# Kernel tuning notes

Hardware: AMD Instinct MI355X
Metric: run time of the kernel (lower is better)

## Reference

```python
import jax, jax.numpy as jnp
import numpy as np

N_NODES = 100000
N_EDGES = 1600000
D_IN = 64
D_OUT = 64
K_PLUS = 3
ALPHA = 0.5
EXPONENT = -0.25


def _dir_norm_edge_weights(row, col, n, exponent):
    # directed_norm: D_out^exp A D_in^exp, zero-degree -> 0 weight
    ones = jnp.ones(row.shape[0], dtype=jnp.float32)
    out_deg = jax.ops.segment_sum(ones, row, num_segments=n)
    in_deg = jax.ops.segment_sum(ones, col, num_segments=n)
    out_inv = jnp.where(out_deg > 0, jnp.power(jnp.maximum(out_deg, 1.0), exponent), 0.0)
    in_inv = jnp.where(in_deg > 0, jnp.power(jnp.maximum(in_deg, 1.0), exponent), 0.0)
    return out_inv[row] * in_inv[col]


def _spmm(w, x, out_idx, gather_idx, n):
    # y[out_idx] += w * x[gather_idx]
    return jax.ops.segment_sum(w[:, None] * x[gather_idx], out_idx, num_segments=n)


def setup_inputs() -> dict:
    key = jax.random.key(0)
    ks = jax.random.split(key, 7)
    x_real = jax.random.normal(ks[0], (N_NODES, D_IN), dtype=jnp.float32)
    x_imag = jax.random.normal(ks[1], (N_NODES, D_IN), dtype=jnp.float32)
    edge_index = jax.random.randint(ks[2], (2, N_EDGES), 0, N_NODES, dtype=jnp.int32)
    s = 1.0 / np.sqrt(D_IN)
    W_real = jax.random.normal(ks[3], (K_PLUS, D_OUT, D_IN), dtype=jnp.float32) * s
    b_real = jax.random.normal(ks[4], (K_PLUS, D_OUT), dtype=jnp.float32) * s
    W_imag = jax.random.normal(ks[5], (K_PLUS, D_OUT, D_IN), dtype=jnp.float32) * s
    b_imag = jax.random.normal(ks[6], (K_PLUS, D_OUT), dtype=jnp.float32) * s
    return {"x_real": x_real, "x_imag": x_imag, "edge_index": edge_index,
            "W_real": W_real, "b_real": b_real, "W_imag": W_imag, "b_imag": b_imag}


def reference(x_real, x_imag, edge_index, W_real, b_real, W_imag, b_imag):
    n = x_real.shape[0]
    row, col = edge_index[0], edge_index[1]
    # adj_norm edge weights; adj_t_norm weights are identical scalars per edge
    # (in/out degrees swap under transpose), only the scatter direction differs.
    w = _dir_norm_edge_weights(row, col, n, EXPONENT)

    y_real = _spmm(w, x_real, row, col, n)    # adj_norm @ x_real
    y_imag = _spmm(w, x_imag, row, col, n)    # adj_norm @ x_imag
    y_real_t = _spmm(w, x_real, col, row, n)  # adj_t_norm @ x_real
    y_imag_t = _spmm(w, x_imag, col, row, n)  # adj_t_norm @ x_imag

    def lin_r(y):  # [K, N, O] per-order real linear
        return jnp.einsum('nd,kod->kno', y, W_real) + b_real[:, None, :]

    def lin_i(y):
        return jnp.einsum('nd,kod->kno', y, W_imag) + b_imag[:, None, :]

    coeffs = (0.5 ** jnp.arange(K_PLUS, dtype=jnp.float32))[:, None, None]  # exp penalty, i=0 -> 1

    lr_yr, li_yr = lin_r(y_real), lin_i(y_real)
    lr_yi, li_yi = lin_r(y_imag), lin_i(y_imag)
    lr_yrt, li_yrt = lin_r(y_real_t), lin_i(y_real_t)
    lr_yit, li_yit = lin_r(y_imag_t), lin_i(y_imag_t)

    sum_real_s2d = jnp.sum((lr_yr - li_yi) * coeffs, axis=0)
    sum_imag_s2d = jnp.sum((li_yr + lr_yi) * coeffs, axis=0)
    sum_real_d2s = jnp.sum((lr_yrt - li_yit) * coeffs, axis=0)
    # NOTE: faithful to original source, which uses y_real (not y_real_t) here.
    sum_imag_d2s = jnp.sum((li_yr + lr_yit) * coeffs, axis=0)

    total_real = ALPHA * sum_real_s2d + (1.0 - ALPHA) * sum_real_d2s
    total_imag = ALPHA * sum_imag_s2d + (1.0 - ALPHA) * sum_imag_d2s
    return total_real, total_imag
```

## Files before the change

### kernel.cpp

```cpp
#include <hip/hip_runtime.h>
#include <hip/hip_fp16.h>


constexpr int D = 64;
constexpr int G1 = 256;

typedef _Float16 f16x8 __attribute__((ext_vector_type(8)));
typedef float f32x4 __attribute__((ext_vector_type(4)));

__device__ __forceinline__ float2 h2_to_f2(uint p) {
  __half2 h = *(__half2*)&p;
  return __half22float2(h);
}


__global__ __launch_bounds__(256) void part_count(
    const int* __restrict__ row, const int* __restrict__ col,
    int* __restrict__ Tcnt, int E, int NBUK, int CH) {
  __shared__ int ho[256], hi_[256];
  int t = threadIdx.x, g = blockIdx.x;
  ho[t] = 0;
  hi_[t] = 0;
  __syncthreads();
  int e0 = g * CH, e1 = min(E, e0 + CH);
  for (int e = e0 + t; e < e1; e += 256) {
    atomicAdd(&ho[row[e] >> 9], 1);
    atomicAdd(&hi_[col[e] >> 9], 1);
  }
  __syncthreads();
  if (t < NBUK) {
    if (ho[t]) atomicAdd(&Tcnt[t], ho[t]);
    if (hi_[t]) atomicAdd(&Tcnt[NBUK + t], hi_[t]);
  }
}

__global__ __launch_bounds__(1024) void prep_kernel(
    const float* __restrict__ Wr, const float* __restrict__ br,
    const float* __restrict__ Wi, const float* __restrict__ bi,
    const int* __restrict__ Tcnt, uint4* __restrict__ Bfrag,
    float* __restrict__ cR, float* __restrict__ cI,
    int* __restrict__ Bb_out, int* __restrict__ Bb_in, int* __restrict__ Ccur,
    int E, int NBUK) {
  __shared__ uint sWh[4096];
  __shared__ int ws[8];
  int t = threadIdx.x;
  for (int i = t; i < 4096; i += 1024) {
    int o = i >> 6, d = i & 63;
    float wr = Wr[i] + 0.5f * Wr[4096 + i] + 0.25f * Wr[8192 + i];
    float wi = Wi[i] + 0.5f * Wi[4096 + i] + 0.25f * Wi[8192 + i];
    __half2 h = __floats2half2_rn(wr, wi);
    sWh[d * 64 + o] = *(uint*)&h;
  }
  if (t < 64) {
    float brv = br[t] + 0.5f * br[64 + t] + 0.25f * br[128 + t];
    float biv = bi[t] + 0.5f * bi[64 + t] + 0.25f * bi[128 + t];
    cR[t] = brv - biv;
    cI[t] = brv + biv;
  }
  int dir = 0, tl = 0, v = 0, sc = 0;
  int lane = t & 63, wv = t >> 6;
  if (t < 512) {
    dir = t >> 8;
    tl = t & 255;
    v = (tl < NBUK) ? Tcnt[dir * NBUK + tl] : 0;
    sc = v;
#pragma unroll
    for (int off = 1; off < 64; off <<= 1) {
      int u = __shfl_up(sc, off);
      if (lane >= off) sc += u;
    }
    if (lane == 63) ws[wv] = sc;
  }
  __syncthreads();
  if (t < 512) {
    int wbase = 0;
#pragma unroll
    for (int w = 0; w < 8; ++w)
      if (w >= (dir << 2) && w < wv) wbase += ws[w];
    int excl = wbase + sc - v;
    int* Bb = dir ? Bb_in : Bb_out;
    if (tl < NBUK) {
      Bb[tl] = excl;
      Ccur[dir * NBUK + tl] = excl;
      if (tl == NBUK - 1) Bb[NBUK] = excl + v;
    }
  }
  for (int tt = t; tt < 2048; tt += 1024) {
    int ln = tt & 63, fr = tt >> 6;
    int mat = fr >> 4, kt = (fr >> 2) & 3, nt = fr & 3;
    int o = (ln & 15) + 16 * nt;
    int k0 = 8 * (ln >> 4) + 32 * kt;
    uint wbits[4];
#pragma unroll
    for (int jj = 0; jj < 4; ++jj) {
      float vv[2];
#pragma unroll
      for (int s = 0; s < 2; ++s) {
        int k = k0 + 2 * jj + s;
        float2 wrwi = h2_to_f2(sWh[(k & 63) * 64 + o]);
        vv[s] = (k < 64) ? wrwi.x : (mat ? wrwi.y : -wrwi.y);
      }
      __half2 hh = __floats2half2_rn(vv[0], vv[1]);
      wbits[jj] = *(uint*)&hh;
    }
    Bfrag[tt] = make_uint4(wbits[0], wbits[1], wbits[2], wbits[3]);
  }
}

__global__ __launch_bounds__(256) void part_scatter(
    const int* __restrict__ row, const int* __restrict__ col,
    int* __restrict__ Ccur,
    uint* __restrict__ pout, uint* __restrict__ pin, int E, int NBUK, int CH) {
  __shared__ int co[256], ci[256];
  int t = threadIdx.x, g = blockIdx.x;
  co[t] = 0;
  ci[t] = 0;
  __syncthreads();
  int e0 = g * CH, e1 = min(E, e0 + CH);
  for (int e = e0 + t; e < e1; e += 256) {
    atomicAdd(&co[row[e] >> 9], 1);
    atomicAdd(&ci[col[e] >> 9], 1);
  }
  __syncthreads();
  if (t < NBUK) {
    int c = co[t];
    co[t] = c ? atomicAdd(&Ccur[t], c) : 0;
    c = ci[t];
    ci[t] = c ? atomicAdd(&Ccur[NBUK + t], c) : 0;
  }
  __syncthreads();
  for (int e = e0 + t; e < e1; e += 256) {
    int r = row[e], c = col[e];
    int po = atomicAdd(&co[r >> 9], 1);
    pout[po] = ((uint)(r & 511) << 17) | (uint)c;
    int pi = atomicAdd(&ci[c >> 9], 1);
    pin[pi] = ((uint)(c & 511) << 17) | (uint)r;
  }
}

__global__ __launch_bounds__(256) void offsets_kernel(
    const uint* __restrict__ pout, const uint* __restrict__ pin,
    const int* __restrict__ Bb_out, const int* __restrict__ Bb_in,
    int* __restrict__ ofs_out, int* __restrict__ ofs_in,
    float* __restrict__ inv_out, float* __restrict__ inv_in,
    int E, int NBUK, int N) {
  const uint* p = blockIdx.y ? pin : pout;
  const int* Bb = blockIdx.y ? Bb_in : Bb_out;
  int* ofs = blockIdx.y ? ofs_in : ofs_out;
  float* inv = blockIdx.y ? inv_in : inv_out;
  __shared__ int ld[512];
  __shared__ int ws[4];
  int t = threadIdx.x, b = blockIdx.x;
  ld[t] = 0;
  ld[t + 256] = 0;
  __syncthreads();
  int win_s = Bb[b], win_e = Bb[b + 1];
  for (int j = win_s + t; j < win_e; j += 256) atomicAdd(&ld[p[j] >> 17], 1);
  __syncthreads();
  int a0 = ld[2 * t], a1 = ld[2 * t + 1], sm = a0 + a1;
  int lane = t & 63, wv = t >> 6, sc = sm;
#pragma unroll
  for (int off = 1; off < 64; off <<= 1) {
    int u = __shfl_up(sc, off);
    if (lane >= off) sc += u;
  }
  if (lane == 63) ws[wv] = sc;
  __syncthreads();
  int wbase = 0;
#pragma unroll
  for (int w = 0; w < 4; ++w)
    if (w < wv) wbase += ws[w];
  int excl = wbase + sc - sm;
  int n0 = (b << 9) + 2 * t;
  if (n0 < N) {
    ofs[n0] = win_s + excl;
    inv[n0] = a0 ? rsqrtf(sqrtf((float)a0)) : 0.0f;
  }
  if (n0 + 1 < N) {
    ofs[n0 + 1] = win_s + excl + a0;
    inv[n0 + 1] = a1 ? rsqrtf(sqrtf((float)a1)) : 0.0f;
  }
  if (b == 0 && t == 0) ofs[N] = E;
}

__global__ __launch_bounds__(256) void bucket_fill(
    const uint* __restrict__ pout, const uint* __restrict__ pin,
    const int* __restrict__ Bb_out, const int* __restrict__ Bb_in,
    const int* __restrict__ ofs_out, const int* __restrict__ ofs_in,
    const float* __restrict__ inv_out, const float* __restrict__ inv_in,
    uint* __restrict__ idx_out, uint* __restrict__ idx_in, int E, int NBUK, int N) {
  const uint* p = blockIdx.y ? pin : pout;
  const int* Bb = blockIdx.y ? Bb_in : Bb_out;
  const int* ofs = blockIdx.y ? ofs_in : ofs_out;
  const float* invnb = blockIdx.y ? inv_out : inv_in;
  uint* idx = blockIdx.y ? idx_in : idx_out;
  __shared__ int cur[512];
  int t = threadIdx.x, b = blockIdx.x;
  int n0 = (b << 9) + t;
  cur[t] = (n0 < N) ? ofs[n0] : 0;
  cur[t + 256] = (n0 + 256 < N) ? ofs[n0 + 256] : 0;
  __syncthreads();
  int s = Bb[b], e = Bb[b + 1];
  for (int j = s + t; j < e; j += 256) {
    uint pk = p[j];
    uint nbr = pk & 0x1FFFFu;
    uint hb = (uint)__half_as_ushort(__float2half(invnb[nbr]));
    int pos = atomicAdd(&cur[pk >> 17], 1);
    idx[pos] = (hb << 17) | nbr;
  }
}


__global__ void pack_kernel(const float* __restrict__ xr, const float* __restrict__ xi,
                            uint* __restrict__ xp, int total4) {
  int i = blockIdx.x * blockDim.x + threadIdx.x;
  if (i < total4) {
    float4 a = ((const float4*)xr)[i];
    float4 b = ((const float4*)xi)[i];
    __half2 h;
    uint4 o;
    h = __floats2half2_rn(a.x, b.x); o.x = *(uint*)&h;
    h = __floats2half2_rn(a.y, b.y); o.y = *(uint*)&h;
    h = __floats2half2_rn(a.z, b.z); o.z = *(uint*)&h;
    h = __floats2half2_rn(a.w, b.w); o.w = *(uint*)&h;
    ((uint4*)xp)[i] = o;
  }
}

__global__ __launch_bounds__(256) void gather_kernel(
    const uint4* __restrict__ xp4,
    const uint* __restrict__ idx_out, const uint* __restrict__ idx_in,
    const int* __restrict__ ofs_out, const int* __restrict__ ofs_in,
    const float* __restrict__ inv_out, const float* __restrict__ inv_in,
    uint* __restrict__ Apack, int N) {
  int wv = threadIdx.x >> 6;
  int lane = threadIdx.x & 63;
  int sub = lane >> 4;
  int q = lane & 15;
  int wid = blockIdx.x * 4 + wv;
  int nw = gridDim.x * 4;
  for (int n = wid; n < N; n += nw) {
    float4 u1 = {0, 0, 0, 0}, s1 = {0, 0, 0, 0};
    float4 v2 = {0, 0, 0, 0}, s2 = {0, 0, 0, 0};
#define ACC(P, SC, U, S)                                                \
  {                                                                     \
    float2 a0 = h2_to_f2((P).x), a1 = h2_to_f2((P).y);                  \
    float2 a2 = h2_to_f2((P).z), a3 = h2_to_f2((P).w);                  \
    U.x += SC * a0.x; S.x += SC * a0.y; U.y += SC * a1.x; S.y += SC * a1.y; \
    U.z += SC * a2.x; S.z += SC * a2.y; U.w += SC * a3.x; S.w += SC * a3.y; \
  }
#define DEC(E) __half2float(__ushort_as_half((ushort)((E) >> 17)))
    {
      int lo = ofs_out[n], hi = ofs_out[n + 1];
      int len8 = (hi - lo) & ~7;
      int j = lo;
      for (; j < lo + len8; j += 8) {
        uint e0 = idx_out[j + sub];
        uint e1 = idx_out[j + 4 + sub];
        uint4 p0 = xp4[(size_t)(e0 & 0x1FFFFu) * 16 + q];
        uint4 p1 = xp4[(size_t)(e1 & 0x1FFFFu) * 16 + q];
        float sc0 = DEC(e0), sc1 = DEC(e1);
        ACC(p0, sc0, u1, s1);
        ACC(p1, sc1, u1, s1);
      }
      for (; j < hi; j += 4) {
        if (j + sub < hi) {
          uint e0 = idx_out[j + sub];
          uint4 p0 = xp4[(size_t)(e0 & 0x1FFFFu) * 16 + q];
          float sc0 = DEC(e0);
          ACC(p0, sc0, u1, s1);
        }
      }
    }
    {
      int lo = ofs_in[n], hi = ofs_in[n + 1];
      int len8 = (hi - lo) & ~7;
      int j = lo;
      for (; j < lo + len8; j += 8) {
        uint e0 = idx_in[j + sub];
        uint e1 = idx_in[j + 4 + sub];
        uint4 p0 = xp4[(size_t)(e0 & 0x1FFFFu) * 16 + q];
        uint4 p1 = xp4[(size_t)(e1 & 0x1FFFFu) * 16 + q];
        float sc0 = DEC(e0), sc1 = DEC(e1);
        ACC(p0, sc0, v2, s2);
        ACC(p1, sc1, v2, s2);
      }
      for (; j < hi; j += 4) {
        if (j + sub < hi) {
          uint e0 = idx_in[j + sub];
          uint4 p0 = xp4[(size_t)(e0 & 0x1FFFFu) * 16 + q];
          float sc0 = DEC(e0);
          ACC(p0, sc0, v2, s2);
        }
      }
    }
#undef ACC
#undef DEC
#pragma unroll
    for (int m = 16; m < 64; m <<= 1) {
      u1.x += __shfl_xor(u1.x, m); u1.y += __shfl_xor(u1.y, m);
      u1.z += __shfl_xor(u1.z, m); u1.w += __shfl_xor(u1.w, m);
      s1.x += __shfl_xor(s1.x, m); s1.y += __shfl_xor(s1.y, m);
      s1.z += __shfl_xor(s1.z, m); s1.w += __shfl_xor(s1.w, m);
      v2.x += __shfl_xor(v2.x, m); v2.y += __shfl_xor(v2.y, m);
      v2.z += __shfl_xor(v2.z, m); v2.w += __shfl_xor(v2.w, m);
      s2.x += __shfl_xor(s2.x, m); s2.y += __shfl_xor(s2.y, m);
      s2.z += __shfl_xor(s2.z, m); s2.w += __shfl_xor(s2.w, m);
    }
    if (sub == 0) {
      float io = inv_out[n], ii = inv_in[n];
      float4 uu = make_float4(io * u1.x, io * u1.y, io * u1.z, io * u1.w);
      float4 vv = make_float4(ii * v2.x, ii * v2.y, ii * v2.z, ii * v2.w);
      float4 ss = make_float4(io * s1.x + ii * s2.x, io * s1.y + ii * s2.y,
                              io * s1.z + ii * s2.z, io * s1.w + ii * s2.w);
      uint* base = Apack + (size_t)n * 96 + 2 * q;
      __half2 h;
      uint2 w;
      h = __floats2half2_rn(0.5f * (uu.x + vv.x), 0.5f * (uu.y + vv.y)); w.x = *(uint*)&h;
      h = __floats2half2_rn(0.5f * (uu.z + vv.z), 0.5f * (uu.w + vv.w)); w.y = *(uint*)&h;
      *(uint2*)base = w;
      h = __floats2half2_rn(0.5f * ss.x, 0.5f * ss.y); w.x = *(uint*)&h;
      h = __floats2half2_rn(0.5f * ss.z, 0.5f * ss.w); w.y = *(uint*)&h;
      *(uint2*)(base + 32) = w;
      h = __floats2half2_rn(uu.x, uu.y); w.x = *(uint*)&h;
      h = __floats2half2_rn(uu.z, uu.w); w.y = *(uint*)&h;
      *(uint2*)(base + 64) = w;
    }
  }
}

__global__ __launch_bounds__(256) void gemm_kernel(
    const ushort* __restrict__ Apack, const uint4* __restrict__ Bfrag,
    const float* __restrict__ cR, const float* __restrict__ cI,
    float* __restrict__ out_real, float* __restrict__ out_imag, int N) {
  __shared__ uint4 sB[2048];
  for (int i = threadIdx.x; i < 2048; i += 256) sB[i] = Bfrag[i];
  __syncthreads();
  int lane = threadIdx.x & 63, wv = threadIdx.x >> 6;
  int l15 = lane & 15, l4 = lane >> 4;
  float bR[4], bI[4];
#pragma unroll
  for (int nt = 0; nt < 4; ++nt) {
    bR[nt] = cR[l15 + 16 * nt];
    bI[nt] = cI[l15 + 16 * nt];
  }
  int tiles = (N + 15) >> 4;
  int gw = blockIdx.x * 4 + wv, nw = gridDim.x * 4;
  for (int tt = gw; tt < tiles; tt += nw) {
    int n0 = tt << 4;
    int arow = min(n0 + l15, N - 1);
    const ushort* ap = Apack + (size_t)arow * 192 + 8 * l4;
    f16x8 a[6];
#pragma unroll
    for (int kt = 0; kt < 6; ++kt) a[kt] = *(const f16x8*)(ap + 32 * kt);
    f32x4 cr[4], ci[4];
#pragma unroll
    for (int nt = 0; nt < 4; ++nt) {
      cr[nt] = (f32x4){0.f, 0.f, 0.f, 0.f};
      ci[nt] = (f32x4){0.f, 0.f, 0.f, 0.f};
    }
#pragma unroll
    for (int kt = 0; kt < 4; ++kt) {
#pragma unroll
      for (int nt = 0; nt < 4; ++nt) {
        f16x8 b0 = *(const f16x8*)&sB[(kt * 4 + nt) * 64 + lane];
        cr[nt] = __builtin_amdgcn_mfma_f32_16x16x32_f16(a[kt], b0, cr[nt], 0, 0, 0);
        f16x8 b1 = *(const f16x8*)&sB[(16 + kt * 4 + nt) * 64 + lane];
        ci[nt] = __builtin_amdgcn_mfma_f32_16x16x32_f16(a[kt + 2], b1, ci[nt], 0, 0, 0);
      }
    }
#pragma unroll
    for (int nt = 0; nt < 4; ++nt) {
#pragma unroll
      for (int r = 0; r < 4; ++r) {
        int node = n0 + 4 * l4 + r;
        if (node < N) {
          out_real[(size_t)node * 64 + l15 + 16 * nt] = cr[nt][r] + bR[nt];
          out_imag[(size_t)node * 64 + l15 + 16 * nt] = ci[nt][r] + bI[nt];
        }
      }
    }
  }
}

extern "C" void kernel_launch(void* const* d_in, const int* in_sizes, int n_in,
                              void* d_out, int out_size, void* d_ws, size_t ws_size,
                              hipStream_t stream) {
  const float* x_real = (const float*)d_in[0];
  const float* x_imag = (const float*)d_in[1];
  const int* edge = (const int*)d_in[2];
  const float* W_real = (const float*)d_in[3];
  const float* b_real = (const float*)d_in[4];
  const float* W_imag = (const float*)d_in[5];
  const float* b_imag = (const float*)d_in[6];

  const int N = in_sizes[0] / D;
  const int E = in_sizes[2] / 2;
  const int* row = edge;
  const int* col = edge + E;

  const int NBUK = (N + 511) >> 9;
  const int CH = (E + G1 - 1) / G1;

  uint* xp       = (uint*)d_ws;
  uint* idx_out  = xp + (size_t)N * D;
  uint* idx_in   = idx_out + E;
  uint* Apack    = idx_in + E;
  uint* pout     = Apack;
  uint* pin      = pout + E;
  uint4* Bfrag   = (uint4*)(Apack + (size_t)N * 96);
  int* Tcnt      = (int*)(Bfrag + 2048);
  int* Bb_out    = Tcnt + 2 * NBUK;
  int* Bb_in     = Bb_out + NBUK + 1;
  int* Ccur      = Bb_in + NBUK + 1;
  int* ofs_out   = Ccur + 2 * NBUK;
  int* ofs_in    = ofs_out + N + 1;
  float* inv_out = (float*)(ofs_in + N + 1);
  float* inv_in  = inv_out + N;
  float* cR      = inv_in + N;
  float* cI      = cR + 64;

  float* out_real = (float*)d_out;
  float* out_imag = out_real + (size_t)N * D;

  hipMemsetAsync(Tcnt, 0, 2 * NBUK * sizeof(int), stream);
  part_count<<<G1, 256, 0, stream>>>(row, col, Tcnt, E, NBUK, CH);

  prep_kernel<<<1, 1024, 0, stream>>>(W_real, b_real, W_imag, b_imag, Tcnt,
                                      Bfrag, cR, cI, Bb_out, Bb_in, Ccur, E, NBUK);

  pack_kernel<<<(N * 16 + 255) / 256, 256, 0, stream>>>(x_real, x_imag, xp, N * 16);

  part_scatter<<<G1, 256, 0, stream>>>(row, col, Ccur, pout, pin, E, NBUK, CH);

  offsets_kernel<<<dim3(NBUK, 2), 256, 0, stream>>>(pout, pin, Bb_out, Bb_in,
                                                    ofs_out, ofs_in, inv_out, inv_in,
                                                    E, NBUK, N);

  bucket_fill<<<dim3(NBUK, 2), 256, 0, stream>>>(pout, pin, Bb_out, Bb_in,
                                                 ofs_out, ofs_in, inv_out, inv_in,
                                                 idx_out, idx_in, E, NBUK, N);

  gather_kernel<<<4096, 256, 0, stream>>>((const uint4*)xp, idx_out, idx_in,
                                          ofs_out, ofs_in, inv_out, inv_in, Apack, N);
  gemm_kernel<<<512, 256, 0, stream>>>((const ushort*)Apack, Bfrag, cR, cI,
                                       out_real, out_imag, N);
}
```

Baseline: 344.1 us.

## Vectorize edge partitioning loads, pad bucket counters, and widen grids

The edge counting and scatter passes now load row/col as int4 and unroll the per-edge atomics. The count pass becomes grid-stride over 1024 blocks and the scatter pass uses 500 blocks with 4-aligned chunks. Global bucket counters are padded to one per 64-byte slot to cut atomic contention from false sharing. The offset and fill passes unroll by four to expose more loads in flight, and the GEMM grid grows to 1568 blocks. The scatter chunking assumes E is divisible by 4 and that chunk boundaries stay 4-aligned, otherwise edges could be double-counted or run past the end.

```diff
diff --git a/kernel.cpp b/kernel.cpp
--- a/kernel.cpp
+++ b/kernel.cpp
@@ -3,7 +3,7 @@
 
 
 constexpr int D = 64;
-constexpr int G1 = 256;
+constexpr int GSC = 500;
 
 typedef _Float16 f16x8 __attribute__((ext_vector_type(8)));
 typedef float f32x4 __attribute__((ext_vector_type(4)));
@@ -16,21 +16,35 @@
 
 __global__ __launch_bounds__(256) void part_count(
     const int* __restrict__ row, const int* __restrict__ col,
-    int* __restrict__ Tcnt, int E, int NBUK, int CH) {
+    int* __restrict__ Tcnt, int E, int NBUK) {
   __shared__ int ho[256], hi_[256];
-  int t = threadIdx.x, g = blockIdx.x;
+  int t = threadIdx.x;
   ho[t] = 0;
   hi_[t] = 0;
   __syncthreads();
-  int e0 = g * CH, e1 = min(E, e0 + CH);
-  for (int e = e0 + t; e < e1; e += 256) {
+  int E4 = E >> 2;
+  int stride = gridDim.x * 256;
+  for (int gi = blockIdx.x * 256 + t; gi < E4; gi += stride) {
+    int4 r4 = ((const int4*)row)[gi];
+    int4 c4 = ((const int4*)col)[gi];
+    atomicAdd(&ho[r4.x >> 9], 1);
+    atomicAdd(&ho[r4.y >> 9], 1);
+    atomicAdd(&ho[r4.z >> 9], 1);
+    atomicAdd(&ho[r4.w >> 9], 1);
+    atomicAdd(&hi_[c4.x >> 9], 1);
+    atomicAdd(&hi_[c4.y >> 9], 1);
+    atomicAdd(&hi_[c4.z >> 9], 1);
+    atomicAdd(&hi_[c4.w >> 9], 1);
+  }
+  if (blockIdx.x == 0 && t < (E & 3)) {
+    int e = (E & ~3) + t;
     atomicAdd(&ho[row[e] >> 9], 1);
     atomicAdd(&hi_[col[e] >> 9], 1);
   }
   __syncthreads();
   if (t < NBUK) {
-    if (ho[t]) atomicAdd(&Tcnt[t], ho[t]);
-    if (hi_[t]) atomicAdd(&Tcnt[NBUK + t], hi_[t]);
+    if (ho[t]) atomicAdd(&Tcnt[t << 4], ho[t]);
+    if (hi_[t]) atomicAdd(&Tcnt[(NBUK + t) << 4], hi_[t]);
   }
 }
 
@@ -62,7 +76,7 @@
   if (t < 512) {
     dir = t >> 8;
     tl = t & 255;
-    v = (tl < NBUK) ? Tcnt[dir * NBUK + tl] : 0;
+    v = (tl < NBUK) ? Tcnt[(dir * NBUK + tl) << 4] : 0;
     sc = v;
 #pragma unroll
     for (int off = 1; off < 64; off <<= 1) {
@@ -81,7 +95,7 @@
     int* Bb = dir ? Bb_in : Bb_out;
     if (tl < NBUK) {
       Bb[tl] = excl;
-      Ccur[dir * NBUK + tl] = excl;
+      Ccur[(dir * NBUK + tl) << 4] = excl;
       if (tl == NBUK - 1) Bb[NBUK] = excl + v;
     }
   }
@@ -117,24 +131,42 @@
   ci[t] = 0;
   __syncthreads();
   int e0 = g * CH, e1 = min(E, e0 + CH);
-  for (int e = e0 + t; e < e1; e += 256) {
-    atomicAdd(&co[row[e] >> 9], 1);
-    atomicAdd(&ci[col[e] >> 9], 1);
+  int g0 = e0 >> 2, g1 = (e1 + 3) >> 2;
+  for (int gi = g0 + t; gi < g1; gi += 256) {
+    int4 r4 = ((const int4*)row)[gi];
+    int4 c4 = ((const int4*)col)[gi];
+    atomicAdd(&co[r4.x >> 9], 1);
+    atomicAdd(&co[r4.y >> 9], 1);
+    atomicAdd(&co[r4.z >> 9], 1);
+    atomicAdd(&co[r4.w >> 9], 1);
+    atomicAdd(&ci[c4.x >> 9], 1);
+    atomicAdd(&ci[c4.y >> 9], 1);
+    atomicAdd(&ci[c4.z >> 9], 1);
+    atomicAdd(&ci[c4.w >> 9], 1);
   }
   __syncthreads();
   if (t < NBUK) {
     int c = co[t];
-    co[t] = c ? atomicAdd(&Ccur[t], c) : 0;
+    co[t] = c ? atomicAdd(&Ccur[t << 4], c) : 0;
     c = ci[t];
-    ci[t] = c ? atomicAdd(&Ccur[NBUK + t], c) : 0;
-  }
-  __syncthreads();
-  for (int e = e0 + t; e < e1; e += 256) {
-    int r = row[e], c = col[e];
-    int po = atomicAdd(&co[r >> 9], 1);
-    pout[po] = ((uint)(r & 511) << 17) | (uint)c;
-    int pi = atomicAdd(&ci[c >> 9], 1);
-    pin[pi] = ((uint)(c & 511) << 17) | (uint)r;
+    ci[t] = c ? atomicAdd(&Ccur[(NBUK + t) << 4], c) : 0;
+  }
+  __syncthreads();
+  for (int gi = g0 + t; gi < g1; gi += 256) {
+    int4 r4 = ((const int4*)row)[gi];
+    int4 c4 = ((const int4*)col)[gi];
+#define SCAT1(R, C)                                          \
+  {                                                          \
+    int po = atomicAdd(&co[(R) >> 9], 1);                    \
+    pout[po] = ((uint)((R) & 511) << 17) | (uint)(C);        \
+    int pi = atomicAdd(&ci[(C) >> 9], 1);                    \
+    pin[pi] = ((uint)((C) & 511) << 17) | (uint)(R);         \
+  }
+    SCAT1(r4.x, c4.x);
+    SCAT1(r4.y, c4.y);
+    SCAT1(r4.z, c4.z);
+    SCAT1(r4.w, c4.w);
+#undef SCAT1
   }
 }
 
@@ -155,7 +187,15 @@
   ld[t + 256] = 0;
   __syncthreads();
   int win_s = Bb[b], win_e = Bb[b + 1];
-  for (int j = win_s + t; j < win_e; j += 256) atomicAdd(&ld[p[j] >> 17], 1);
+  int j = win_s + t;
+  for (; j + 768 < win_e; j += 1024) {
+    uint p0 = p[j], p1 = p[j + 256], p2 = p[j + 512], p3 = p[j + 768];
+    atomicAdd(&ld[p0 >> 17], 1);
+    atomicAdd(&ld[p1 >> 17], 1);
+    atomicAdd(&ld[p2 >> 17], 1);
+    atomicAdd(&ld[p3 >> 17], 1);
+  }
+  for (; j < win_e; j += 256) atomicAdd(&ld[p[j] >> 17], 1);
   __syncthreads();
   int a0 = ld[2 * t], a1 = ld[2 * t + 1], sm = a0 + a1;
   int lane = t & 63, wv = t >> 6, sc = sm;
@@ -201,13 +241,26 @@
   cur[t + 256] = (n0 + 256 < N) ? ofs[n0 + 256] : 0;
   __syncthreads();
   int s = Bb[b], e = Bb[b + 1];
-  for (int j = s + t; j < e; j += 256) {
+#define FILL1(PK)                                                       \
+  {                                                                     \
+    uint nbr = (PK) & 0x1FFFFu;                                         \
+    uint hb = (uint)__half_as_ushort(__float2half(invnb[nbr]));         \
+    int pos = atomicAdd(&cur[(PK) >> 17], 1);                           \
+    idx[pos] = (hb << 17) | nbr;                                        \
+  }
+  int j = s + t;
+  for (; j + 768 < e; j += 1024) {
+    uint p0 = p[j], p1 = p[j + 256], p2 = p[j + 512], p3 = p[j + 768];
+    FILL1(p0);
+    FILL1(p1);
+    FILL1(p2);
+    FILL1(p3);
+  }
+  for (; j < e; j += 256) {
     uint pk = p[j];
-    uint nbr = pk & 0x1FFFFu;
-    uint hb = (uint)__half_as_ushort(__float2half(invnb[nbr]));
-    int pos = atomicAdd(&cur[pk >> 17], 1);
-    idx[pos] = (hb << 17) | nbr;
-  }
+    FILL1(pk);
+  }
+#undef FILL1
 }
 
 
@@ -400,7 +453,7 @@
   const int* col = edge + E;
 
   const int NBUK = (N + 511) >> 9;
-  const int CH = (E + G1 - 1) / G1;
+  const int CH = ((E / GSC + 3) & ~3);
 
   uint* xp       = (uint*)d_ws;
   uint* idx_out  = xp + (size_t)N * D;
@@ -410,10 +463,10 @@
   uint* pin      = pout + E;
   uint4* Bfrag   = (uint4*)(Apack + (size_t)N * 96);
   int* Tcnt      = (int*)(Bfrag + 2048);
-  int* Bb_out    = Tcnt + 2 * NBUK;
+  int* Ccur      = Tcnt + 2 * NBUK * 16;
+  int* Bb_out    = Ccur + 2 * NBUK * 16;
   int* Bb_in     = Bb_out + NBUK + 1;
-  int* Ccur      = Bb_in + NBUK + 1;
-  int* ofs_out   = Ccur + 2 * NBUK;
+  int* ofs_out   = Bb_in + NBUK + 1;
   int* ofs_in    = ofs_out + N + 1;
   float* inv_out = (float*)(ofs_in + N + 1);
   float* inv_in  = inv_out + N;
@@ -423,15 +476,15 @@
   float* out_real = (float*)d_out;
   float* out_imag = out_real + (size_t)N * D;
 
-  hipMemsetAsync(Tcnt, 0, 2 * NBUK * sizeof(int), stream);
-  part_count<<<G1, 256, 0, stream>>>(row, col, Tcnt, E, NBUK, CH);
+  hipMemsetAsync(Tcnt, 0, 2 * NBUK * 16 * sizeof(int), stream);
+  part_count<<<1024, 256, 0, stream>>>(row, col, Tcnt, E, NBUK);
 
   prep_kernel<<<1, 1024, 0, stream>>>(W_real, b_real, W_imag, b_imag, Tcnt,
                                       Bfrag, cR, cI, Bb_out, Bb_in, Ccur, E, NBUK);
 
   pack_kernel<<<(N * 16 + 255) / 256, 256, 0, stream>>>(x_real, x_imag, xp, N * 16);
 
-  part_scatter<<<G1, 256, 0, stream>>>(row, col, Ccur, pout, pin, E, NBUK, CH);
+  part_scatter<<<GSC, 256, 0, stream>>>(row, col, Ccur, pout, pin, E, NBUK, CH);
 
   offsets_kernel<<<dim3(NBUK, 2), 256, 0, stream>>>(pout, pin, Bb_out, Bb_in,
                                                     ofs_out, ofs_in, inv_out, inv_in,
@@ -443,6 +496,6 @@
 
   gather_kernel<<<4096, 256, 0, stream>>>((const uint4*)xp, idx_out, idx_in,
                                           ofs_out, ofs_in, inv_out, inv_in, Apack, N);
-  gemm_kernel<<<512, 256, 0, stream>>>((const ushort*)Apack, Bfrag, cR, cI,
-                                       out_real, out_imag, N);
-}
+  gemm_kernel<<<1568, 256, 0, stream>>>((const ushort*)Apack, Bfrag, cR, cI,
+                                        out_real, out_imag, N);
+}
```

Measured after the change: 346.3 us. Within noise of the previous version (+0.6%).
